# Kernel optimization log

Measured on AMD Instinct MI355X. Metric: run time of the kernel, lower is better.

## Reference

```python
import jax, jax.numpy as jnp
import numpy as np

IGNORE_INDEX = -100


def setup_inputs() -> dict:
    key = jax.random.key(0)
    k_e, k_c, k_t = jax.random.split(key, 3)
    N, D, V = 8192, 1024, 50257
    e = jax.random.normal(k_e, (N, D), dtype=jnp.float32)
    c = jax.random.normal(k_c, (V, D), dtype=jnp.float32)
    targets = jax.random.randint(k_t, (N,), 0, V, dtype=jnp.int64)
    return {"e": e, "c": c, "targets": targets}


def reference(e, c, targets):
    # Fused linear projection + cross entropy (logits never kept beyond this op
    # in the original CCE kernel; here we express the same math directly).
    # e: [N, D], c: [V, D], targets: [N]
    valid = targets != IGNORE_INDEX
    safe_t = jnp.where(valid, targets, 0)

    # logits [N, V] -- the huge intermediate CCE tiles away
    logits = jnp.einsum("nd,vd->nv", e, c)
    lse = jax.nn.logsumexp(logits, axis=-1)                    # [N]
    tgt_logit = jnp.take_along_axis(logits, safe_t[:, None], axis=-1)[:, 0]

    nll = jnp.where(valid, lse - tgt_logit, 0.0)
    n_valid = jnp.maximum(jnp.sum(valid.astype(jnp.float32)), 1.0)
    return jnp.sum(nll) / n_valid  # reduction='mean' over non-ignored tokens
```

## Files before the change

### kernel.cpp

```cpp
#include <hip/hip_runtime.h>
#include <hip/hip_bf16.h>
#include <math.h>

#define IGNORE_INDEX (-100)

constexpr int N = 8192;
constexpr int D = 1024;
constexpr int V = 50257;

constexpr int BM = 128;
constexpr int BN = 256;
constexpr int BK = 128;
constexpr int NC = 16;
constexpr int SUBT = (V + BN - 1) / BN;

constexpr float LOG2E = 1.44269504088896340736f;
constexpr float LN2 = 0.69314718055994530942f;

typedef __attribute__((ext_vector_type(8))) int int8v;
typedef __attribute__((ext_vector_type(4))) float floatx4;

__device__ __forceinline__ void gload_lds16(const void* g, void* l) {
  __builtin_amdgcn_global_load_lds(
      (const __attribute__((address_space(1))) void*)g,
      (__attribute__((address_space(3))) void*)l, 16, 0, 0);
}

__device__ __forceinline__ float fexp2(float x) {
#if __has_builtin(__builtin_amdgcn_exp2f)
  return __builtin_amdgcn_exp2f(x);
#else
  return exp2f(x);
#endif
}

constexpr int E8 = N * D / 8;
constexpr int C8 = V * D / 8;
constexpr int EB = E8 / 256;
constexpr int CB = (C8 + 255) / 256;
constexpr int TGT_BLOCKS = N / 4;

__device__ __forceinline__ unsigned int pk4_fp8(float a, float b, float c,
                                                float d) {
  int p = __builtin_amdgcn_cvt_pk_fp8_f32(a, b, 0, false);
  p = __builtin_amdgcn_cvt_pk_fp8_f32(c, d, p, true);
  return (unsigned int)p;
}

__global__ void prep_kernel(const float* __restrict__ e,
                            const float* __restrict__ c,
                            const int* __restrict__ t,
                            unsigned int* __restrict__ e8,
                            unsigned int* __restrict__ c8,
                            float* __restrict__ tgt) {
  const int b = blockIdx.x;
  if (b < EB) {
    const int idx = b * 256 + threadIdx.x;
    const float4 v0 = ((const float4*)e)[idx * 2];
    const float4 v1 = ((const float4*)e)[idx * 2 + 1];
    uint2 o;
    o.x = pk4_fp8(v0.x * LOG2E, v0.y * LOG2E, v0.z * LOG2E, v0.w * LOG2E);
    o.y = pk4_fp8(v1.x * LOG2E, v1.y * LOG2E, v1.z * LOG2E, v1.w * LOG2E);
    ((uint2*)e8)[idx] = o;
  } else if (b < EB + CB) {
    const int idx = (b - EB) * 256 + threadIdx.x;
    if (idx < C8) {
      const float4 v0 = ((const float4*)c)[idx * 2];
      const float4 v1 = ((const float4*)c)[idx * 2 + 1];
      uint2 o;
      o.x = pk4_fp8(v0.x, v0.y, v0.z, v0.w);
      o.y = pk4_fp8(v1.x, v1.y, v1.z, v1.w);
      ((uint2*)c8)[idx] = o;
    }
  } else {
    const int row = (b - EB - CB) * 4 + (threadIdx.x >> 6);
    const int lane = threadIdx.x & 63;
    int tr = t[row];
    if (tr == IGNORE_INDEX) tr = 0;
    const float4* ev = (const float4*)(e + (size_t)row * D);
    const float4* cv = (const float4*)(c + (size_t)tr * D);
    float s = 0.f;
#pragma unroll
    for (int k = 0; k < 4; ++k) {
      float4 a = ev[lane + k * 64];
      float4 bb = cv[lane + k * 64];
      s += a.x * bb.x + a.y * bb.y + a.z * bb.z + a.w * bb.w;
    }
#pragma unroll
    for (int d = 1; d < 64; d <<= 1) s += __shfl_xor(s, d, 64);
    if (lane == 0) tgt[row] = s;
  }
}

__global__ __launch_bounds__(256, 2) void gemm_lse_kernel(
    const unsigned char* __restrict__ A, const unsigned char* __restrict__ B,
    float* __restrict__ m_part, float* __restrict__ s_part) {
  __shared__ char smB[2][BN * BK];
  __shared__ float red_m[2][BM];
  __shared__ float red_s[2][BM];

  const int chunk = blockIdx.x;
  const int row0 = blockIdx.y * BM;
  const int tid = threadIdx.x;
  const int wave = tid >> 6;
  const int lane = tid & 63;
  const int wr = wave >> 1;
  const int wc = wave & 1;
  const int quad = lane >> 4;
  const int l16 = lane & 15;

  const int lrow = lane >> 3;
  const int lvec_st = (lane & 7) ^ lrow;

  const int4* abase =
      (const int4*)(A + (size_t)(row0 + wr * 64 + l16) * D + quad * 32);

  float rm[16], rs[16];
#pragma unroll
  for (int x = 0; x < 16; ++x) { rm[x] = -1e30f; rs[x] = 0.0f; }

  const int nsub = (SUBT - chunk + NC - 1) / NC;

  {
    const int col0 = chunk * BN;
#pragma unroll
    for (int cc = 0; cc < 8; ++cc) {
      const int ch = wave * 8 + cc;
      int brow = col0 + ch * 8 + lrow;
      if (brow >= V) brow = V - 1;
      gload_lds16(B + (size_t)brow * D + lvec_st * 16,
                  smB[0] + ch * 1024 + lane * 16);
    }
  }
  __syncthreads();

  int cur = 0;
  for (int si = 0; si < nsub; ++si) {
    const int col0 = (chunk + si * NC) * BN;
    floatx4 acc[4][8];
#pragma unroll
    for (int i = 0; i < 4; ++i)
#pragma unroll
      for (int j = 0; j < 8; ++j) acc[i][j] = floatx4{0.f, 0.f, 0.f, 0.f};

#pragma unroll 1
    for (int ks = 0; ks < D / BK; ++ks) {
      const char* bufR = smB[cur];
      char* bufW = smB[cur ^ 1];

      int8v af[4];
#pragma unroll
      for (int i = 0; i < 4; ++i) {
        const int4 lo = abase[i * 1024 + ks * 8];
        const int4 hi = abase[i * 1024 + ks * 8 + 1];
        af[i][0] = lo.x; af[i][1] = lo.y; af[i][2] = lo.z; af[i][3] = lo.w;
        af[i][4] = hi.x; af[i][5] = hi.y; af[i][6] = hi.z; af[i][7] = hi.w;
      }

      if (!(si == nsub - 1 && ks == 7)) {
        const int ksn = (ks + 1) & 7;
        const int col0n = (ks == 7) ? col0 + NC * BN : col0;
#pragma unroll
        for (int cc = 0; cc < 8; ++cc) {
          const int ch = wave * 8 + cc;
          int brow = col0n + ch * 8 + lrow;
          if (brow >= V) brow = V - 1;
          gload_lds16(B + (size_t)brow * D + ksn * BK + lvec_st * 16,
                      bufW + ch * 1024 + lane * 16);
        }
      }

#pragma unroll
      for (int jh = 0; jh < 2; ++jh) {
        int8v bf[4];
#pragma unroll
        for (int jj = 0; jj < 4; ++jj) {
          const int cr = wc * 128 + (jh * 4 + jj) * 16 + l16;
          const char* base = bufR + cr * 128;
          const int4 lo =
              *(const int4*)(base + (((quad * 2) ^ (cr & 7)) * 16));
          const int4 hi =
              *(const int4*)(base + (((quad * 2 + 1) ^ (cr & 7)) * 16));
          bf[jj][0] = lo.x; bf[jj][1] = lo.y; bf[jj][2] = lo.z; bf[jj][3] = lo.w;
          bf[jj][4] = hi.x; bf[jj][5] = hi.y; bf[jj][6] = hi.z; bf[jj][7] = hi.w;
        }
#pragma unroll
        for (int jj = 0; jj < 4; ++jj)
#pragma unroll
          for (int i = 0; i < 4; ++i)
            acc[i][jh * 4 + jj] =
                __builtin_amdgcn_mfma_scale_f32_16x16x128_f8f6f4(
                    af[i], bf[jj], acc[i][jh * 4 + jj], 0, 0,
                    0, 0x7F7F7F7F, 0, 0x7F7F7F7F);
      }

      __syncthreads();
      cur ^= 1;
    }

    {
      const bool edge = (col0 + BN > V);
#pragma unroll
      for (int i = 0; i < 4; ++i) {
#pragma unroll
        for (int reg = 0; reg < 4; ++reg) {
          float v[8];
#pragma unroll
          for (int j = 0; j < 8; ++j) v[j] = acc[i][j][reg];
          if (edge) {
            const int cb = col0 + wc * 128 + l16;
#pragma unroll
            for (int j = 0; j < 8; ++j)
              if (cb + j * 16 >= V) v[j] = -INFINITY;
          }
          float mx = v[0];
#pragma unroll
          for (int j = 1; j < 8; ++j) mx = fmaxf(mx, v[j]);
          const int x = i * 4 + reg;
          const float nm = fmaxf(rm[x], mx);
          float s = rs[x] * fexp2(rm[x] - nm);
#pragma unroll
          for (int j = 0; j < 8; ++j) s += fexp2(v[j] - nm);
          rs[x] = s;
          rm[x] = nm;
        }
      }
    }
  }

#pragma unroll
  for (int x = 0; x < 16; ++x) {
    float m = rm[x], s = rs[x];
#pragma unroll
    for (int d = 1; d < 16; d <<= 1) {
      const float om = __shfl_xor(m, d, 64);
      const float os = __shfl_xor(s, d, 64);
      const float nm = fmaxf(m, om);
      s = s * fexp2(m - nm) + os * fexp2(om - nm);
      m = nm;
    }
    if (l16 == 0) {
      const int i = x >> 2, reg = x & 3;
      const int rloc = wr * 64 + i * 16 + quad * 4 + reg;
      red_m[wc][rloc] = m;
      red_s[wc][rloc] = s;
    }
  }
  __syncthreads();
  if (tid < BM) {
    const float m0 = red_m[0][tid], s0 = red_s[0][tid];
    const float m1 = red_m[1][tid], s1 = red_s[1][tid];
    const float tm = fmaxf(m0, m1);
    const float ts = s0 * fexp2(m0 - tm) + s1 * fexp2(m1 - tm);
    m_part[(size_t)chunk * N + row0 + tid] = tm;
    s_part[(size_t)chunk * N + row0 + tid] = ts;
  }
}

__global__ void finalize1_kernel(const float* __restrict__ m_part,
                                 const float* __restrict__ s_part,
                                 const float* __restrict__ tgt,
                                 const int* __restrict__ t,
                                 double* __restrict__ fin) {
  const int tid = threadIdx.x;
  const int row = blockIdx.x * 256 + tid;
  float M = -1e30f;
#pragma unroll
  for (int ch = 0; ch < NC; ++ch) M = fmaxf(M, m_part[ch * N + row]);
  float S = 0.f;
#pragma unroll
  for (int ch = 0; ch < NC; ++ch)
    S += s_part[ch * N + row] * fexp2(m_part[ch * N + row] - M);
  const float lse = LN2 * (M + log2f(S));
  double nll = 0.0;
  double cnt = 0.0;
  if (t[row] != IGNORE_INDEX) {
    nll = (double)(lse - tgt[row]);
    cnt = 1.0;
  }
  __shared__ double sacc[256];
  __shared__ double scnt[256];
  sacc[tid] = nll;
  scnt[tid] = cnt;
  __syncthreads();
  for (int s = 128; s > 0; s >>= 1) {
    if (tid < s) {
      sacc[tid] += sacc[tid + s];
      scnt[tid] += scnt[tid + s];
    }
    __syncthreads();
  }
  if (tid == 0) {
    fin[blockIdx.x * 2] = sacc[0];
    fin[blockIdx.x * 2 + 1] = scnt[0];
  }
}

__global__ void finalize2_kernel(const double* __restrict__ fin,
                                 float* __restrict__ out) {
  const int tid = threadIdx.x;
  __shared__ double sa[64], sc[64];
  sa[tid] = (tid < 32) ? fin[tid * 2] : 0.0;
  sc[tid] = (tid < 32) ? fin[tid * 2 + 1] : 0.0;
  __syncthreads();
  for (int s = 32; s > 0; s >>= 1) {
    if (tid < s) {
      sa[tid] += sa[tid + s];
      sc[tid] += sc[tid + s];
    }
    __syncthreads();
  }
  if (tid == 0) out[0] = (float)(sa[0] / fmax(sc[0], 1.0));
}

extern "C" void kernel_launch(void* const* d_in, const int* in_sizes, int n_in,
                              void* d_out, int out_size, void* d_ws,
                              size_t ws_size, hipStream_t stream) {
  const float* e = (const float*)d_in[0];
  const float* c = (const float*)d_in[1];
  const int* t = (const int*)d_in[2];
  float* out = (float*)d_out;

  char* ws = (char*)d_ws;
  unsigned char* e8 = (unsigned char*)ws;
  size_t off = (size_t)N * D;
  unsigned char* c8 = (unsigned char*)(ws + off);
  off += (size_t)V * D;
  off = (off + 255) & ~(size_t)255;
  float* tgt = (float*)(ws + off);
  off += (size_t)N * 4;
  float* m_part = (float*)(ws + off);
  off += (size_t)NC * N * 4;
  float* s_part = (float*)(ws + off);
  off += (size_t)NC * N * 4;
  double* fin = (double*)(ws + off);
  off += 32 * 2 * sizeof(double);

  prep_kernel<<<EB + CB + TGT_BLOCKS, 256, 0, stream>>>(
      e, c, t, (unsigned int*)e8, (unsigned int*)c8, tgt);
  gemm_lse_kernel<<<dim3(NC, N / BM), 256, 0, stream>>>(e8, c8, m_part,
                                                        s_part);
  finalize1_kernel<<<32, 256, 0, stream>>>(m_part, s_part, tgt, t, fin);
  finalize2_kernel<<<1, 64, 0, stream>>>(fin, out);
}
```

Measured before the change: 881.3 us.

## Software-pipeline A register loads and B LDS staging with explicit waitcnt barriers

Restructures the K loop so the next step's B tile (global-to-LDS) and A fragments (global-to-register) are issued before the current MFMA block. Partial vmcnt waits replace full __syncthreads, letting the prefetched loads overlap compute. It also raises wave priority around the MFMA bursts. The cost is extra registers for the double-buffered A fragments, and the hand-placed waitcnt counts make correctness fragile. The last iteration now issues one extra clamped prefetch that is never used.

After: 1.601 ms. +81.7%, slower.

```diff
diff --git a/kernel.cpp b/kernel.cpp
--- a/kernel.cpp
+++ b/kernel.cpp
@@ -121,18 +121,29 @@
 
   const int nsub = (SUBT - chunk + NC - 1) / NC;
 
-  {
-    const int col0 = chunk * BN;
+  auto stage = [&](int col0s, int kss, char* dst) {
 #pragma unroll
     for (int cc = 0; cc < 8; ++cc) {
       const int ch = wave * 8 + cc;
-      int brow = col0 + ch * 8 + lrow;
+      int brow = col0s + ch * 8 + lrow;
       if (brow >= V) brow = V - 1;
-      gload_lds16(B + (size_t)brow * D + lvec_st * 16,
-                  smB[0] + ch * 1024 + lane * 16);
-    }
-  }
-  __syncthreads();
+      gload_lds16(B + (size_t)brow * D + kss * BK + lvec_st * 16,
+                  dst + ch * 1024 + lane * 16);
+    }
+  };
+  auto loadA = [&](int kss, int8v* af) {
+#pragma unroll
+    for (int i = 0; i < 4; ++i) {
+      const int4 lo = abase[i * 1024 + kss * 8];
+      const int4 hi = abase[i * 1024 + kss * 8 + 1];
+      af[i][0] = lo.x; af[i][1] = lo.y; af[i][2] = lo.z; af[i][3] = lo.w;
+      af[i][4] = hi.x; af[i][5] = hi.y; af[i][6] = hi.z; af[i][7] = hi.w;
+    }
+  };
+
+  stage(chunk * BN, 0, smB[0]);
+  int8v af[4];
+  loadA(0, af);
 
   int cur = 0;
   for (int si = 0; si < nsub; ++si) {
@@ -145,31 +156,19 @@
 
 #pragma unroll 1
     for (int ks = 0; ks < D / BK; ++ks) {
+      const int ksn = (ks + 1) & 7;
+      const int col0n = (ks == 7) ? col0 + NC * BN : col0;
+
+      stage(col0n, ksn, smB[cur ^ 1]);
+      int8v afn[4];
+      loadA(ksn, afn);
+
+      __builtin_amdgcn_sched_barrier(0);
+      asm volatile("s_waitcnt vmcnt(16)" ::: "memory");
+      __builtin_amdgcn_sched_barrier(0);
+      __builtin_amdgcn_s_barrier();
+
       const char* bufR = smB[cur];
-      char* bufW = smB[cur ^ 1];
-
-      int8v af[4];
-#pragma unroll
-      for (int i = 0; i < 4; ++i) {
-        const int4 lo = abase[i * 1024 + ks * 8];
-        const int4 hi = abase[i * 1024 + ks * 8 + 1];
-        af[i][0] = lo.x; af[i][1] = lo.y; af[i][2] = lo.z; af[i][3] = lo.w;
-        af[i][4] = hi.x; af[i][5] = hi.y; af[i][6] = hi.z; af[i][7] = hi.w;
-      }
-
-      if (!(si == nsub - 1 && ks == 7)) {
-        const int ksn = (ks + 1) & 7;
-        const int col0n = (ks == 7) ? col0 + NC * BN : col0;
-#pragma unroll
-        for (int cc = 0; cc < 8; ++cc) {
-          const int ch = wave * 8 + cc;
-          int brow = col0n + ch * 8 + lrow;
-          if (brow >= V) brow = V - 1;
-          gload_lds16(B + (size_t)brow * D + ksn * BK + lvec_st * 16,
-                      bufW + ch * 1024 + lane * 16);
-        }
-      }
-
 #pragma unroll
       for (int jh = 0; jh < 2; ++jh) {
         int8v bf[4];
@@ -184,6 +183,7 @@
           bf[jj][0] = lo.x; bf[jj][1] = lo.y; bf[jj][2] = lo.z; bf[jj][3] = lo.w;
           bf[jj][4] = hi.x; bf[jj][5] = hi.y; bf[jj][6] = hi.z; bf[jj][7] = hi.w;
         }
+        __builtin_amdgcn_s_setprio(1);
 #pragma unroll
         for (int jj = 0; jj < 4; ++jj)
 #pragma unroll
@@ -192,9 +192,16 @@
                 __builtin_amdgcn_mfma_scale_f32_16x16x128_f8f6f4(
                     af[i], bf[jj], acc[i][jh * 4 + jj], 0, 0,
                     0, 0x7F7F7F7F, 0, 0x7F7F7F7F);
+        __builtin_amdgcn_s_setprio(0);
       }
 
-      __syncthreads();
+#pragma unroll
+      for (int i = 0; i < 4; ++i) af[i] = afn[i];
+      if (ks != 7) {
+        asm volatile("s_waitcnt lgkmcnt(0)" ::: "memory");
+        __builtin_amdgcn_sched_barrier(0);
+        __builtin_amdgcn_s_barrier();
+      }
       cur ^= 1;
     }
 
@@ -226,6 +233,9 @@
         }
       }
     }
+    asm volatile("s_waitcnt lgkmcnt(0)" ::: "memory");
+    __builtin_amdgcn_sched_barrier(0);
+    __builtin_amdgcn_s_barrier();
   }
 
 #pragma unroll
```
